# Kernel optimization log

Measured on AMD Instinct MI355X. Metric: run time of the kernel, lower is better.

Reference implementation:

```python
import jax, jax.numpy as jnp
import numpy as np

N, M = 8192, 128
EPS = 1e-4


def setup_inputs() -> dict:
    key = jax.random.key(0)
    k1, k2, k3 = jax.random.split(key, 3)
    out1 = jax.random.normal(k1, (N, M), dtype=jnp.float32)
    out2 = jax.random.normal(k2, (N, M), dtype=jnp.float32)
    label = jax.random.uniform(k3, (N, N), dtype=jnp.float32)
    return {"out1": out1, "out2": out2, "label": label}


def _dir_loss(a, b, mob):
    # pairwise_inner_product(a, b) in the torch code equals b @ a.T:
    # inner[i, j] = <b[i], a[j]>
    scores = jnp.einsum('im,jm->ij', b, a)          # [n, n]
    phat = jax.nn.softmax(scores, axis=-1)
    return jnp.sum(-mob * jnp.log(phat + EPS))


def reference(out1, out2, label):
    loss = _dir_loss(out1, out2, label)
    loss = loss + _dir_loss(out2, out1, label.T)
    return loss
```

## Files before the change

### kernel.cpp

```cpp
#include <hip/hip_runtime.h>
#include <hip/hip_bf16.h>
#include <stdint.h>

#define NN 8192
#define MM 128
#define EPSF 1e-4f
#define SHIFT 30.0f

typedef __bf16 bf16x8 __attribute__((ext_vector_type(8)));
typedef float floatx4 __attribute__((ext_vector_type(4)));

__device__ __forceinline__ void pf16(const float* g, void* lds) {
    __builtin_amdgcn_global_load_lds(
        (__attribute__((address_space(1))) void*)(uintptr_t)g,
        (__attribute__((address_space(3))) void*)(uint32_t)(uintptr_t)lds,
        16, 0, 0);
}

#define CVT8(dst, ptr)                                                        \
    do {                                                                      \
        float4 v0_ = *reinterpret_cast<const float4*>(ptr);                   \
        float4 v1_ = *reinterpret_cast<const float4*>((ptr) + 4);             \
        bf16x8 t_ = { (__bf16)v0_.x, (__bf16)v0_.y, (__bf16)v0_.z,            \
                      (__bf16)v0_.w, (__bf16)v1_.x, (__bf16)v1_.y,            \
                      (__bf16)v1_.z, (__bf16)v1_.w };                         \
        dst = t_;                                                             \
    } while (0)

__global__ __launch_bounds__(256)
void sums_kernel(const float* __restrict__ A, const float* __restrict__ B,
                 const float* __restrict__ label, float* __restrict__ sums,
                 float* __restrict__ out) {
    __shared__ alignas(16) __bf16 Bs[2][64 * 128];
    __shared__ alignas(16) char pfbuf[1024];
    const int tid = threadIdx.x;
    const int w = tid >> 6, lane = tid & 63, q = lane >> 4, ln = lane & 15;
    const int i0 = blockIdx.y * 256 + w * 64;
    const int jbase = blockIdx.x * 256;
    const int bid = blockIdx.y * gridDim.x + blockIdx.x;
    const float* pfb = label + (size_t)bid * 32768 + w * 8192 + lane * 4;

    if (bid == 0 && tid == 0) *out = 0.f;

    const floatx4 accInit = {-SHIFT, -SHIFT, -SHIFT, -SHIFT};

    bf16x8 a[4][4];
    #pragma unroll
    for (int rg = 0; rg < 4; ++rg) {
        const float* ap = A + (size_t)(i0 + rg * 16 + ln) * MM + q * 8;
        #pragma unroll
        for (int k = 0; k < 4; ++k)
            CVT8(a[rg][k], ap + k * 32);
    }

#define STAGE(dstbuf, js_)                                                    \
    do {                                                                      \
        const float* srcb_ = B + (size_t)(jbase + (js_) * 64) * MM;           \
        char* d_ = reinterpret_cast<char*>(dstbuf);                           \
        _Pragma("unroll")                                                     \
        for (int u_ = 0; u_ < 4; ++u_) {                                      \
            int ch_ = u_ * 256 + tid;                                         \
            int row_ = ch_ >> 4, slot_ = ch_ & 15;                            \
            bf16x8 t2_;                                                       \
            CVT8(t2_, srcb_ + row_ * MM + slot_ * 8);                         \
            *reinterpret_cast<bf16x8*>(                                       \
                d_ + row_ * 256 + ((slot_ ^ (row_ & 7)) << 4)) = t2_;         \
        }                                                                     \
    } while (0)

    float p[4][4];
    #pragma unroll
    for (int rg = 0; rg < 4; ++rg)
        #pragma unroll
        for (int r = 0; r < 4; ++r) p[rg][r] = 0.f;

    STAGE(Bs[0], 0);
    int buf = 0;
    for (int js = 0; js < 4; ++js) {
        __syncthreads();
        if (js < 3) STAGE(Bs[buf ^ 1], js + 1);
        #pragma unroll
        for (int u = 0; u < 8; ++u)
            pf16(pfb + js * 2048 + u * 256, pfbuf);

        const int j0 = jbase + js * 64;
        const char* bsc = reinterpret_cast<const char*>(Bs[buf]);
        const int sw = ln & 7;
        #pragma unroll
        for (int cg = 0; cg < 4; ++cg) {
            const char* bp = bsc + (cg * 16 + ln) * 256;
            bf16x8 b[4];
            #pragma unroll
            for (int k = 0; k < 4; ++k)
                b[k] = *reinterpret_cast<const bf16x8*>(bp + (((q + 4 * k) ^ sw) << 4));
            floatx4 acc[4] = {accInit, accInit, accInit, accInit};
            #pragma unroll
            for (int k = 0; k < 4; ++k)
                #pragma unroll
                for (int rg = 0; rg < 4; ++rg)
                    acc[rg] = __builtin_amdgcn_mfma_f32_16x16x32_bf16(a[rg][k], b[k], acc[rg], 0, 0, 0);
            float c = 0.f;
            #pragma unroll
            for (int rg = 0; rg < 4; ++rg) {
                float e[4];
                #pragma unroll
                for (int r = 0; r < 4; ++r) {
                    e[r] = __expf(acc[rg][r]);
                    p[rg][r] += e[r];
                }
                c += (e[0] + e[1]) + (e[2] + e[3]);
            }
            c += __shfl_xor(c, 16);
            c += __shfl_xor(c, 32);
            if (q == 0) atomicAdd(&sums[NN + j0 + cg * 16 + ln], c);
        }
        buf ^= 1;
    }
#undef STAGE

    #pragma unroll
    for (int m = 1; m <= 8; m <<= 1)
        #pragma unroll
        for (int rg = 0; rg < 4; ++rg)
            #pragma unroll
            for (int r = 0; r < 4; ++r)
                p[rg][r] += __shfl_xor(p[rg][r], m);
    if (ln == 0)
        #pragma unroll
        for (int rg = 0; rg < 4; ++rg)
            #pragma unroll
            for (int r = 0; r < 4; ++r)
                atomicAdd(&sums[i0 + rg * 16 + q * 4 + r], p[rg][r]);
}

__global__ __launch_bounds__(256)
void loss_kernel(const float* __restrict__ A, const float* __restrict__ B,
                 const float* __restrict__ sums, const float* __restrict__ label,
                 float* __restrict__ out) {
    __shared__ alignas(16) __bf16 Bs[128 * 128];
    __shared__ float Rr[128], Rc[128];
    __shared__ float red[4];
    const int tid = threadIdx.x;
    const int w = tid >> 6, lane = tid & 63, q = lane >> 4, ln = lane & 15;
    const int i0 = blockIdx.y * 128 + w * 32;
    const int jbase = blockIdx.x * 128;

    const float* labp[2] = {
        label + (size_t)(i0 + ln) * NN + jbase,
        label + (size_t)(i0 + 16 + ln) * NN + jbase
    };
    floatx4 lb[2][2][4];
    #pragma unroll
    for (int js = 0; js < 2; ++js)
        #pragma unroll
        for (int cg = 0; cg < 4; ++cg) {
            const int c4 = js * 64 + cg * 16 + q * 4;
            lb[js][0][cg] = *reinterpret_cast<const floatx4*>(&labp[0][c4]);
            lb[js][1][cg] = *reinterpret_cast<const floatx4*>(&labp[1][c4]);
        }

    if (tid < 128) Rr[tid] = 1.0f / sums[blockIdx.y * 128 + tid];
    else           Rc[tid - 128] = 1.0f / sums[NN + jbase + (tid - 128)];

    {
        const float* srcb = B + (size_t)jbase * MM;
        char* d = reinterpret_cast<char*>(Bs);
        #pragma unroll
        for (int u = 0; u < 8; ++u) {
            int ch = u * 256 + tid;
            int row = ch >> 4, slot = ch & 15;
            bf16x8 t;
            CVT8(t, srcb + row * MM + slot * 8);
            *reinterpret_cast<bf16x8*>(d + row * 256 + ((slot ^ (row & 7)) << 4)) = t;
        }
    }

    const floatx4 accInit = {-SHIFT, -SHIFT, -SHIFT, -SHIFT};

    bf16x8 a[2][4];
    #pragma unroll
    for (int rg = 0; rg < 2; ++rg) {
        const float* ap = A + (size_t)(i0 + rg * 16 + ln) * MM + q * 8;
        #pragma unroll
        for (int k = 0; k < 4; ++k)
            CVT8(a[rg][k], ap + k * 32);
    }
    __syncthreads();

    const float rl[2] = { Rr[w * 32 + ln], Rr[w * 32 + 16 + ln] };

    const char* bsc = reinterpret_cast<const char*>(Bs);
    const int sw = ln & 7;
    float lacc = 0.f;
    #pragma unroll
    for (int js = 0; js < 2; ++js) {
        const int j0 = js * 64;
        #pragma unroll
        for (int cg = 0; cg < 4; ++cg) {
            const floatx4 rc = *reinterpret_cast<const floatx4*>(&Rc[j0 + cg * 16 + q * 4]);
            const char* bp = bsc + (j0 + cg * 16 + ln) * 256;
            bf16x8 b[4];
            #pragma unroll
            for (int k = 0; k < 4; ++k)
                b[k] = *reinterpret_cast<const bf16x8*>(bp + (((q + 4 * k) ^ sw) << 4));
            floatx4 acc0 = accInit, acc1 = accInit;
            #pragma unroll
            for (int k = 0; k < 4; ++k) {
                acc0 = __builtin_amdgcn_mfma_f32_16x16x32_bf16(b[k], a[0][k], acc0, 0, 0, 0);
                acc1 = __builtin_amdgcn_mfma_f32_16x16x32_bf16(b[k], a[1][k], acc1, 0, 0, 0);
            }
            #pragma unroll
            for (int r = 0; r < 4; ++r) {
                float e0 = __expf(acc0[r]);
                float t0 = __logf(fmaf(e0, rl[0], EPSF) * fmaf(e0, rc[r], EPSF));
                lacc = fmaf(lb[js][0][cg][r], t0, lacc);
                float e1 = __expf(acc1[r]);
                float t1 = __logf(fmaf(e1, rl[1], EPSF) * fmaf(e1, rc[r], EPSF));
                lacc = fmaf(lb[js][1][cg][r], t1, lacc);
            }
        }
    }

    #pragma unroll
    for (int m = 1; m <= 32; m <<= 1) lacc += __shfl_xor(lacc, m);
    if (lane == 0) red[w] = lacc;
    __syncthreads();
    if (tid == 0) atomicAdd(out, -((red[0] + red[1]) + (red[2] + red[3])));
}

extern "C" void kernel_launch(void* const* d_in, const int* in_sizes, int n_in,
                              void* d_out, int out_size, void* d_ws, size_t ws_size,
                              hipStream_t stream) {
    const float* out1 = (const float*)d_in[0];
    const float* out2 = (const float*)d_in[1];
    const float* label = (const float*)d_in[2];

    float* sums = (float*)d_ws;

    hipMemsetAsync(sums, 0, 2 * NN * sizeof(float), stream);

    sums_kernel<<<dim3(32, 32), 256, 0, stream>>>(out2, out1, label, sums,
                                                  (float*)d_out);

    loss_kernel<<<dim3(64, 64), 256, 0, stream>>>(out2, out1, sums, label,
                                                  (float*)d_out);
}
```

Baseline: 422.4 us.

## Replace global atomics with per-block partial sums and drop memset

Row and column exp-sums are now written as per-block partials to workspace arrays. The loss kernel reduces those 32 partials per row and column, so the global float atomics and the memset launch go away. Column partials are first combined across waves in shared memory. The label prefetch pattern is also changed to walk row bands in the order the loss kernel will read them, which should improve L2 reuse. In exchange, the loss kernel does extra reads of the partial arrays and the workspace grows.

Result: no change. 421.6 us (-0.2%).

```diff
diff --git a/kernel.cpp b/kernel.cpp
--- a/kernel.cpp
+++ b/kernel.cpp
@@ -29,16 +29,20 @@
 
 __global__ __launch_bounds__(256)
 void sums_kernel(const float* __restrict__ A, const float* __restrict__ B,
-                 const float* __restrict__ label, float* __restrict__ sums,
+                 const float* __restrict__ label,
+                 float* __restrict__ rowp, float* __restrict__ colp,
                  float* __restrict__ out) {
     __shared__ alignas(16) __bf16 Bs[2][64 * 128];
+    __shared__ float colw[4][256];
     __shared__ alignas(16) char pfbuf[1024];
     const int tid = threadIdx.x;
     const int w = tid >> 6, lane = tid & 63, q = lane >> 4, ln = lane & 15;
     const int i0 = blockIdx.y * 256 + w * 64;
     const int jbase = blockIdx.x * 256;
     const int bid = blockIdx.y * gridDim.x + blockIdx.x;
-    const float* pfb = label + (size_t)bid * 32768 + w * 8192 + lane * 4;
+    const int band = bid >> 5, sub = bid & 31;
+    const float* pfb = label + (size_t)(band * 256 + sub * 4) * NN
+                       + (size_t)w * NN + lane * 4;
 
     if (bid == 0 && tid == 0) *out = 0.f;
 
@@ -83,7 +87,6 @@
         for (int u = 0; u < 8; ++u)
             pf16(pfb + js * 2048 + u * 256, pfbuf);
 
-        const int j0 = jbase + js * 64;
         const char* bsc = reinterpret_cast<const char*>(Bs[buf]);
         const int sw = ln & 7;
         #pragma unroll
@@ -112,7 +115,7 @@
             }
             c += __shfl_xor(c, 16);
             c += __shfl_xor(c, 32);
-            if (q == 0) atomicAdd(&sums[NN + j0 + cg * 16 + ln], c);
+            if (q == 0) colw[w][js * 64 + cg * 16 + ln] = c;
         }
         buf ^= 1;
     }
@@ -130,13 +133,19 @@
         for (int rg = 0; rg < 4; ++rg)
             #pragma unroll
             for (int r = 0; r < 4; ++r)
-                atomicAdd(&sums[i0 + rg * 16 + q * 4 + r], p[rg][r]);
+                rowp[(size_t)blockIdx.x * NN + i0 + rg * 16 + q * 4 + r] = p[rg][r];
+
+    __syncthreads();
+    {
+        float cs = (colw[0][tid] + colw[1][tid]) + (colw[2][tid] + colw[3][tid]);
+        colp[(size_t)blockIdx.y * NN + jbase + tid] = cs;
+    }
 }
 
 __global__ __launch_bounds__(256)
 void loss_kernel(const float* __restrict__ A, const float* __restrict__ B,
-                 const float* __restrict__ sums, const float* __restrict__ label,
-                 float* __restrict__ out) {
+                 const float* __restrict__ rowp, const float* __restrict__ colp,
+                 const float* __restrict__ label, float* __restrict__ out) {
     __shared__ alignas(16) __bf16 Bs[128 * 128];
     __shared__ float Rr[128], Rc[128];
     __shared__ float red[4];
@@ -159,8 +168,19 @@
             lb[js][1][cg] = *reinterpret_cast<const floatx4*>(&labp[1][c4]);
         }
 
-    if (tid < 128) Rr[tid] = 1.0f / sums[blockIdx.y * 128 + tid];
-    else           Rc[tid - 128] = 1.0f / sums[NN + jbase + (tid - 128)];
+    if (tid < 128) {
+        const int row = blockIdx.y * 128 + tid;
+        float s = 0.f;
+        #pragma unroll 8
+        for (int b = 0; b < 32; ++b) s += rowp[(size_t)b * NN + row];
+        Rr[tid] = 1.0f / s;
+    } else {
+        const int col = jbase + tid - 128;
+        float s = 0.f;
+        #pragma unroll 8
+        for (int b = 0; b < 32; ++b) s += colp[(size_t)b * NN + col];
+        Rc[tid - 128] = 1.0f / s;
+    }
 
     {
         const float* srcb = B + (size_t)jbase * MM;
@@ -235,13 +255,13 @@
     const float* out2 = (const float*)d_in[1];
     const float* label = (const float*)d_in[2];
 
-    float* sums = (float*)d_ws;
-
-    hipMemsetAsync(sums, 0, 2 * NN * sizeof(float), stream);
-
-    sums_kernel<<<dim3(32, 32), 256, 0, stream>>>(out2, out1, label, sums,
-                                                  (float*)d_out);
-
-    loss_kernel<<<dim3(64, 64), 256, 0, stream>>>(out2, out1, sums, label,
-                                                  (float*)d_out);
-}
+    float* rowp = (float*)d_ws;
+    float* colp = rowp + 32 * NN;
+
+
+    sums_kernel<<<dim3(32, 32), 256, 0, stream>>>(out2, out1, label,
+                                                  rowp, colp, (float*)d_out);
+
+    loss_kernel<<<dim3(64, 64), 256, 0, stream>>>(out2, out1, rowp, colp,
+                                                  label, (float*)d_out);
+}
```
